# Performance work log

Measured on AMD Instinct MI355X. Metric: run time of the kernel, lower is better.

The kernel has to match this reference:

```python
import jax, jax.numpy as jnp
import numpy as np

def setup_inputs() -> dict:
    key = jax.random.key(0)
    k1, k2 = jax.random.split(key)
    N, M, D = 4096, 4096, 1024
    set1 = jax.random.normal(k1, (N, D), dtype=jnp.float32)
    set2 = jax.random.normal(k2, (M, D), dtype=jnp.float32)
    return {"set1": set1, "set2": set2}

def _l2_dist(x, y):
    # mean over D of squared differences, computed via the expanded GEMM form
    D = x.shape[-1]
    x2 = jnp.sum(x * x, axis=-1)          # [N]
    y2 = jnp.sum(y * y, axis=-1)          # [M]
    xy = jnp.einsum('nd,md->nm', x, y)    # [N, M]
    return (x2[:, None] - 2.0 * xy + y2[None, :]) / D

def reference(set1, set2):
    dist = _l2_dist(set1, set2)                 # [N, M]
    t1 = jnp.mean(jnp.min(dist, axis=1))        # nearest set2 point per set1 point
    t2 = jnp.mean(jnp.min(dist, axis=0))        # nearest set1 point per set2 point
    return (t1 + t2) * 0.5
```

## Files before the change

### kernel.cpp

```cpp
#include <hip/hip_runtime.h>
#include <hip/hip_bf16.h>
#include <stdint.h>


#define NPTS 4096
#define MPTS 4096
#define DDIM 1024

typedef __attribute__((ext_vector_type(8))) short bf16x8;
typedef __attribute__((ext_vector_type(4))) float f32x4;
typedef __attribute__((ext_vector_type(4))) unsigned short us4;

__device__ __forceinline__ unsigned short f2bf(float f) {
    unsigned int u = __float_as_uint(f);
    unsigned int r = 0x7FFFu + ((u >> 16) & 1u);
    return (unsigned short)((u + r) >> 16);
}

__device__ __forceinline__ void gl_lds16(const void* g, void* l) {
    __builtin_amdgcn_global_load_lds(
        (const __attribute__((address_space(1))) unsigned int*)g,
        (__attribute__((address_space(3))) unsigned int*)l, 16, 0, 0);
}

__global__ __launch_bounds__(256) void prepass_kernel(
    const float* __restrict__ s1, const float* __restrict__ s2,
    unsigned short* __restrict__ b1, unsigned short* __restrict__ b2,
    float* __restrict__ norms, unsigned int* __restrict__ mins) {
    const int row = blockIdx.x * 4 + (threadIdx.x >> 6);
    const int lane = threadIdx.x & 63;
    const float* src;
    unsigned short* dst;
    if (row < NPTS) { src = s1 + (size_t)row * DDIM; dst = b1 + (size_t)row * DDIM; }
    else            { src = s2 + (size_t)(row - NPTS) * DDIM; dst = b2 + (size_t)(row - NPTS) * DDIM; }
    float sq = 0.f;
    #pragma unroll
    for (int i = 0; i < 4; ++i) {
        float4 v = ((const float4*)src)[lane + i * 64];
        sq += v.x * v.x + v.y * v.y + v.z * v.z + v.w * v.w;
        us4 o;
        o.x = f2bf(v.x); o.y = f2bf(v.y); o.z = f2bf(v.z); o.w = f2bf(v.w);
        ((us4*)dst)[lane + i * 64] = o;
    }
    #pragma unroll
    for (int off = 32; off; off >>= 1) sq += __shfl_down(sq, off, 64);
    if (lane == 0) { norms[row] = sq; mins[row] = 0x7f7f7f7fu; }
}


#define STAGE_H(ldsBase, gRowBase, kcol) do {                                   \
    gl_lds16((gRowBase) + (size_t)(wave * 8 + srow) * DDIM + (kcol) + schoff,   \
             ldsb + (ldsBase) + wave * 1024);                                   \
    gl_lds16((gRowBase) + (size_t)(64 + wave * 8 + srow) * DDIM + (kcol) + schoff, \
             ldsb + (ldsBase) + 8192 + wave * 1024);                            \
} while (0)

#define RD_A(CURB, aq) do {                                                     \
    _Pragma("unroll")                                                           \
    for (int fl_ = 0; fl_ < 4; ++fl_) {                                         \
        const int row_ = wr * 128 + (aq) * 64 + fl_ * 16 + r0;                  \
        af[fl_][0] = *(const bf16x8*)(ldsb + (CURB) + row_ * 128 + ch0);        \
        af[fl_][1] = *(const bf16x8*)(ldsb + (CURB) + row_ * 128 + ch1);        \
    }                                                                           \
} while (0)

#define RD_B(CURB, bq, dst) do {                                                \
    _Pragma("unroll")                                                           \
    for (int fj_ = 0; fj_ < 2; ++fj_) {                                         \
        const int col_ = wc * 64 + (bq) * 32 + fj_ * 16 + r0;                   \
        dst[fj_][0] = *(const bf16x8*)(ldsb + (CURB) + 32768 + col_ * 128 + ch0); \
        dst[fj_][1] = *(const bf16x8*)(ldsb + (CURB) + 32768 + col_ * 128 + ch1); \
    }                                                                           \
} while (0)

#define MFMA_Q(aq, bq, BF)                                                      \
    _Pragma("unroll")                                                           \
    for (int fl_ = 0; fl_ < 4; ++fl_) {                                         \
        _Pragma("unroll")                                                       \
        for (int fj_ = 0; fj_ < 2; ++fj_) {                                     \
            acc[(aq) * 4 + fl_][(bq) * 2 + fj_] =                               \
                __builtin_amdgcn_mfma_f32_16x16x32_bf16(af[fl_][0], BF[fj_][0], \
                    acc[(aq) * 4 + fl_][(bq) * 2 + fj_], 0, 0, 0);              \
            acc[(aq) * 4 + fl_][(bq) * 2 + fj_] =                               \
                __builtin_amdgcn_mfma_f32_16x16x32_bf16(af[fl_][1], BF[fj_][1], \
                    acc[(aq) * 4 + fl_][(bq) * 2 + fj_], 0, 0, 0);              \
        }                                                                       \
    }

#define BARRIER_MFMA(aq, bq, BF, WAITSTMT) do {                                 \
    __builtin_amdgcn_s_barrier();                                               \
    asm volatile("s_waitcnt lgkmcnt(0)" ::: "memory");                          \
    __builtin_amdgcn_sched_barrier(0);                                          \
    __builtin_amdgcn_s_setprio(1);                                              \
    MFMA_Q(aq, bq, BF);                                                         \
    __builtin_amdgcn_s_setprio(0);                                              \
    WAITSTMT;                                                                   \
    __builtin_amdgcn_s_barrier();                                               \
} while (0)

#define TILE(t, CURB, NXTB) do {                                                \
    const int kN1_ = ((t) + 1) * 64, kN2_ = ((t) + 2) * 64;                     \
    RD_A(CURB, 0); RD_B(CURB, 0, bf0);                                          \
    if ((t) + 1 < 16) STAGE_H((NXTB) + 49152, Bb + 128 * DDIM, kN1_);           \
    BARRIER_MFMA(0, 0, bf0, );                                                  \
    RD_B(CURB, 1, bf1);                                                         \
    if ((t) + 1 < 16) STAGE_H((NXTB) + 16384, Ab + 128 * DDIM, kN1_);           \
    BARRIER_MFMA(0, 1, bf1, );                                                  \
    RD_A(CURB, 1);                                                              \
    if ((t) + 2 < 16) STAGE_H((CURB) + 32768, Bb, kN2_);                        \
    BARRIER_MFMA(1, 1, bf1, );                                                  \
    if ((t) + 2 < 16) STAGE_H((CURB) + 0, Ab, kN2_);                            \
    BARRIER_MFMA(1, 0, bf0,                                                     \
        if ((t) < 14) { asm volatile("s_waitcnt vmcnt(4)" ::: "memory"); }      \
        else if ((t) == 14) { asm volatile("s_waitcnt vmcnt(0)" ::: "memory"); });\
} while (0)

__global__ __launch_bounds__(512, 2) void cham_gemm_kernel(
    const unsigned short* __restrict__ A,
    const unsigned short* __restrict__ B,
    const float* __restrict__ x2, const float* __restrict__ y2,
    unsigned int* __restrict__ mins,
    unsigned int* __restrict__ ctr, float* __restrict__ out) {
    __shared__ __align__(16) char lds[131072];
    char* ldsb = lds;
    unsigned int* rowmin = mins;
    unsigned int* colmin = mins + NPTS;

    const int g = blockIdx.x;
    const int xcd = g & 7;
    const int s = g >> 3;
    const int bi = (xcd >> 1) * 4 + (s >> 3);
    const int bj = (xcd & 1) * 8 + (s & 7);

    const int tid = threadIdx.x;
    const int wave = tid >> 6;
    const int lane = tid & 63;
    const int wr = wave >> 2;
    const int wc = wave & 3;
    const int r0 = lane & 15;
    const int q = lane >> 4;

    const int ch0 = ((q ^ (r0 & 7)) << 4);
    const int ch1 = (((4 + q) ^ (r0 & 7)) << 4);
    const int srow = lane >> 3;
    const int schoff = (((lane & 7) ^ srow) * 8);

    const unsigned short* Ab = A + (size_t)(bi * 256) * DDIM;
    const unsigned short* Bb = B + (size_t)(bj * 256) * DDIM;

    f32x4 acc[8][4];
    #pragma unroll
    for (int i = 0; i < 8; ++i)
        #pragma unroll
        for (int j = 0; j < 4; ++j)
            acc[i][j] = (f32x4){0.f, 0.f, 0.f, 0.f};

    bf16x8 af[4][2], bf0[2][2], bf1[2][2];

    STAGE_H(0 + 32768, Bb, 0);
    STAGE_H(0 + 0, Ab, 0);
    STAGE_H(0 + 49152, Bb + 128 * DDIM, 0);
    STAGE_H(0 + 16384, Ab + 128 * DDIM, 0);
    STAGE_H(65536 + 32768, Bb, 64);
    STAGE_H(65536 + 0, Ab, 64);
    asm volatile("s_waitcnt vmcnt(4)" ::: "memory");
    __builtin_amdgcn_s_barrier();

    for (int tt = 0; tt < 8; ++tt) {
        const int te = 2 * tt, to = 2 * tt + 1;
        TILE(te, 0, 65536);
        TILE(to, 65536, 0);
    }

    const float invD = 1.0f / (float)DDIM;
    const int nb = bi * 256 + wr * 128;
    const int mb = bj * 256 + wc * 64;

    float y2v[4];
    #pragma unroll
    for (int fj = 0; fj < 4; ++fj)
        y2v[fj] = y2[mb + (fj >> 1) * 32 + (fj & 1) * 16 + r0];

    float cv[4];
    #pragma unroll
    for (int fj = 0; fj < 4; ++fj) cv[fj] = 3.0e38f;

    #pragma unroll
    for (int fi = 0; fi < 8; ++fi) {
        #pragma unroll
        for (int rg = 0; rg < 4; ++rg) {
            const int n = nb + fi * 16 + q * 4 + rg;
            const float x2v = x2[n];
            float rv = 3.0e38f;
            #pragma unroll
            for (int fj = 0; fj < 4; ++fj) {
                float d = (x2v + y2v[fj] - 2.0f * acc[fi][fj][rg]) * invD;
                rv = fminf(rv, d);
                cv[fj] = fminf(cv[fj], d);
            }
            rv = fminf(rv, __shfl_xor(rv, 1, 64));
            rv = fminf(rv, __shfl_xor(rv, 2, 64));
            rv = fminf(rv, __shfl_xor(rv, 4, 64));
            rv = fminf(rv, __shfl_xor(rv, 8, 64));
            if (r0 == 0) atomicMin(&rowmin[n], __float_as_uint(rv));
        }
    }

    #pragma unroll
    for (int fj = 0; fj < 4; ++fj) {
        float v = cv[fj];
        v = fminf(v, __shfl_xor(v, 16, 64));
        v = fminf(v, __shfl_xor(v, 32, 64));
        if (lane < 16)
            atomicMin(&colmin[mb + (fj >> 1) * 32 + (fj & 1) * 16 + lane],
                      __float_as_uint(v));
    }

    __syncthreads();
    __shared__ unsigned int lastflag;
    if (tid == 0)
        lastflag = __hip_atomic_fetch_add(&ctr[0], 1u, __ATOMIC_ACQUIRE,
                                          __HIP_MEMORY_SCOPE_AGENT);
    __syncthreads();
    if (lastflag == 255u) {
        float sum = 0.f;
        #pragma unroll
        for (int i = 0; i < 16; ++i)
            sum += __uint_as_float(__hip_atomic_load(&mins[tid + i * 512],
                    __ATOMIC_RELAXED, __HIP_MEMORY_SCOPE_AGENT));
        #pragma unroll
        for (int off = 32; off; off >>= 1) sum += __shfl_down(sum, off, 64);
        float* red = (float*)(ldsb + 64);
        if (lane == 0) red[wave] = sum;
        __syncthreads();
        if (tid == 0) {
            float tot = 0.f;
            #pragma unroll
            for (int i = 0; i < 8; ++i) tot += red[i];
            out[0] = tot * (1.0f / 8192.0f);
        }
    }
}

extern "C" void kernel_launch(void* const* d_in, const int* in_sizes, int n_in,
                              void* d_out, int out_size, void* d_ws, size_t ws_size,
                              hipStream_t stream) {
    const float* s1 = (const float*)d_in[0];
    const float* s2 = (const float*)d_in[1];
    char* ws = (char*)d_ws;

    unsigned short* b1 = (unsigned short*)ws;
    unsigned short* b2 = (unsigned short*)(ws + 8388608);
    float* norms       = (float*)(ws + 16777216);
    unsigned int* mins = (unsigned int*)(ws + 16777216 + 32768);
    unsigned int* ctr  = (unsigned int*)(ws + 16777216 + 65536);
    float* out = (float*)d_out;

    hipMemsetAsync(ctr, 0, 4, stream);
    prepass_kernel<<<2048, 256, 0, stream>>>(s1, s2, b1, b2, norms, mins);
    cham_gemm_kernel<<<256, 512, 0, stream>>>(b1, b2, norms, norms + NPTS,
                                              mins, ctr, out);
}
```

Measured before the change: 130.4 us.

## Switch GEMM to FP8 MFMA with 128x256 tiles and triple-buffered LDS

Inputs are quantized to FP8 instead of BF16 in the prepass, and the distance GEMM uses fp8 MFMA instructions, halving operand bytes. Block tiles shrink to 128x256 with a three-buffer LDS ring, giving 512 blocks and higher occupancy. The separate memset of the completion counter is folded into the prepass kernel, and the XCD-aware block swizzle is dropped. FP8 quantization of the dot products costs accuracy and may push the result past tolerance.

```diff
diff --git a/kernel.cpp b/kernel.cpp
--- a/kernel.cpp
+++ b/kernel.cpp
@@ -7,15 +7,7 @@
 #define MPTS 4096
 #define DDIM 1024
 
-typedef __attribute__((ext_vector_type(8))) short bf16x8;
 typedef __attribute__((ext_vector_type(4))) float f32x4;
-typedef __attribute__((ext_vector_type(4))) unsigned short us4;
-
-__device__ __forceinline__ unsigned short f2bf(float f) {
-    unsigned int u = __float_as_uint(f);
-    unsigned int r = 0x7FFFu + ((u >> 16) & 1u);
-    return (unsigned short)((u + r) >> 16);
-}
 
 __device__ __forceinline__ void gl_lds16(const void* g, void* l) {
     __builtin_amdgcn_global_load_lds(
@@ -25,22 +17,24 @@
 
 __global__ __launch_bounds__(256) void prepass_kernel(
     const float* __restrict__ s1, const float* __restrict__ s2,
-    unsigned short* __restrict__ b1, unsigned short* __restrict__ b2,
-    float* __restrict__ norms, unsigned int* __restrict__ mins) {
+    unsigned char* __restrict__ a8, unsigned char* __restrict__ b8,
+    float* __restrict__ norms, unsigned int* __restrict__ mins,
+    unsigned int* __restrict__ ctr) {
     const int row = blockIdx.x * 4 + (threadIdx.x >> 6);
     const int lane = threadIdx.x & 63;
+    if (blockIdx.x == 0 && threadIdx.x == 0) ctr[0] = 0u;
     const float* src;
-    unsigned short* dst;
-    if (row < NPTS) { src = s1 + (size_t)row * DDIM; dst = b1 + (size_t)row * DDIM; }
-    else            { src = s2 + (size_t)(row - NPTS) * DDIM; dst = b2 + (size_t)(row - NPTS) * DDIM; }
+    unsigned char* dst;
+    if (row < NPTS) { src = s1 + (size_t)row * DDIM; dst = a8 + (size_t)row * DDIM; }
+    else            { src = s2 + (size_t)(row - NPTS) * DDIM; dst = b8 + (size_t)(row - NPTS) * DDIM; }
     float sq = 0.f;
     #pragma unroll
     for (int i = 0; i < 4; ++i) {
         float4 v = ((const float4*)src)[lane + i * 64];
         sq += v.x * v.x + v.y * v.y + v.z * v.z + v.w * v.w;
-        us4 o;
-        o.x = f2bf(v.x); o.y = f2bf(v.y); o.z = f2bf(v.z); o.w = f2bf(v.w);
-        ((us4*)dst)[lane + i * 64] = o;
+        int p = __builtin_amdgcn_cvt_pk_fp8_f32(v.x, v.y, 0, false);
+        p = __builtin_amdgcn_cvt_pk_fp8_f32(v.z, v.w, p, true);
+        ((int*)dst)[lane + i * 64] = p;
     }
     #pragma unroll
     for (int off = 32; off; off >>= 1) sq += __shfl_down(sq, off, 64);
@@ -48,19 +42,33 @@
 }
 
 
-#define STAGE_H(ldsBase, gRowBase, kcol) do {                                   \
-    gl_lds16((gRowBase) + (size_t)(wave * 8 + srow) * DDIM + (kcol) + schoff,   \
-             ldsb + (ldsBase) + wave * 1024);                                   \
-    gl_lds16((gRowBase) + (size_t)(64 + wave * 8 + srow) * DDIM + (kcol) + schoff, \
-             ldsb + (ldsBase) + 8192 + wave * 1024);                            \
+#define BUF0 0
+#define BUF1 24576
+#define BUF2 49152
+
+#define STAGE_A(bufB, kcol) do {                                                \
+    gl_lds16(Ab + (size_t)(wave * 16 + (lane >> 2)) * DDIM + (kcol)             \
+                 + (((lane & 3) ^ ((lane >> 2) & 3)) * 16),                     \
+             ldsb + (bufB) + wave * 1024);                                      \
+} while (0)
+
+#define STAGE_B1(bufB, kcol) do {                                               \
+    gl_lds16(Bb + (size_t)(wave * 16 + (lane >> 2)) * DDIM + (kcol)             \
+                 + (((lane & 3) ^ ((lane >> 2) & 3)) * 16),                     \
+             ldsb + (bufB) + 8192 + wave * 1024);                               \
+} while (0)
+#define STAGE_B2(bufB, kcol) do {                                               \
+    gl_lds16(Bb + (size_t)(128 + wave * 16 + (lane >> 2)) * DDIM + (kcol)       \
+                 + (((lane & 3) ^ ((lane >> 2) & 3)) * 16),                     \
+             ldsb + (bufB) + 8192 + 8192 + wave * 1024);                        \
 } while (0)
 
 #define RD_A(CURB, aq) do {                                                     \
     _Pragma("unroll")                                                           \
-    for (int fl_ = 0; fl_ < 4; ++fl_) {                                         \
-        const int row_ = wr * 128 + (aq) * 64 + fl_ * 16 + r0;                  \
-        af[fl_][0] = *(const bf16x8*)(ldsb + (CURB) + row_ * 128 + ch0);        \
-        af[fl_][1] = *(const bf16x8*)(ldsb + (CURB) + row_ * 128 + ch1);        \
+    for (int fl_ = 0; fl_ < 2; ++fl_) {                                         \
+        const int row_ = wr * 64 + (aq) * 32 + fl_ * 16 + r0;                   \
+        af[fl_][0] = *(const long*)(ldsb + (CURB) + row_ * 64 + ch0);           \
+        af[fl_][1] = *(const long*)(ldsb + (CURB) + row_ * 64 + ch1);           \
     }                                                                           \
 } while (0)
 
@@ -68,22 +76,22 @@
     _Pragma("unroll")                                                           \
     for (int fj_ = 0; fj_ < 2; ++fj_) {                                         \
         const int col_ = wc * 64 + (bq) * 32 + fj_ * 16 + r0;                   \
-        dst[fj_][0] = *(const bf16x8*)(ldsb + (CURB) + 32768 + col_ * 128 + ch0); \
-        dst[fj_][1] = *(const bf16x8*)(ldsb + (CURB) + 32768 + col_ * 128 + ch1); \
+        dst[fj_][0] = *(const long*)(ldsb + (CURB) + 8192 + col_ * 64 + ch0);   \
+        dst[fj_][1] = *(const long*)(ldsb + (CURB) + 8192 + col_ * 64 + ch1);   \
     }                                                                           \
 } while (0)
 
 #define MFMA_Q(aq, bq, BF)                                                      \
     _Pragma("unroll")                                                           \
-    for (int fl_ = 0; fl_ < 4; ++fl_) {                                         \
+    for (int fl_ = 0; fl_ < 2; ++fl_) {                                         \
         _Pragma("unroll")                                                       \
         for (int fj_ = 0; fj_ < 2; ++fj_) {                                     \
-            acc[(aq) * 4 + fl_][(bq) * 2 + fj_] =                               \
-                __builtin_amdgcn_mfma_f32_16x16x32_bf16(af[fl_][0], BF[fj_][0], \
-                    acc[(aq) * 4 + fl_][(bq) * 2 + fj_], 0, 0, 0);              \
-            acc[(aq) * 4 + fl_][(bq) * 2 + fj_] =                               \
-                __builtin_amdgcn_mfma_f32_16x16x32_bf16(af[fl_][1], BF[fj_][1], \
-                    acc[(aq) * 4 + fl_][(bq) * 2 + fj_], 0, 0, 0);              \
+            acc[(aq) * 2 + fl_][(bq) * 2 + fj_] =                               \
+                __builtin_amdgcn_mfma_f32_16x16x32_fp8_fp8(af[fl_][0], BF[fj_][0], \
+                    acc[(aq) * 2 + fl_][(bq) * 2 + fj_], 0, 0, 0);              \
+            acc[(aq) * 2 + fl_][(bq) * 2 + fj_] =                               \
+                __builtin_amdgcn_mfma_f32_16x16x32_fp8_fp8(af[fl_][1], BF[fj_][1], \
+                    acc[(aq) * 2 + fl_][(bq) * 2 + fj_], 0, 0, 0);              \
         }                                                                       \
     }
 
@@ -99,39 +107,34 @@
 } while (0)
 
 #define TILE(t, CURB, NXTB) do {                                                \
-    const int kN1_ = ((t) + 1) * 64, kN2_ = ((t) + 2) * 64;                     \
+    const int kN_ = ((t) + 2) * 64;                                             \
     RD_A(CURB, 0); RD_B(CURB, 0, bf0);                                          \
-    if ((t) + 1 < 16) STAGE_H((NXTB) + 49152, Bb + 128 * DDIM, kN1_);           \
+    if ((t) + 2 < 16) STAGE_A(NXTB, kN_);                                       \
     BARRIER_MFMA(0, 0, bf0, );                                                  \
     RD_B(CURB, 1, bf1);                                                         \
-    if ((t) + 1 < 16) STAGE_H((NXTB) + 16384, Ab + 128 * DDIM, kN1_);           \
+    if ((t) + 2 < 16) STAGE_B1(NXTB, kN_);                                      \
     BARRIER_MFMA(0, 1, bf1, );                                                  \
     RD_A(CURB, 1);                                                              \
-    if ((t) + 2 < 16) STAGE_H((CURB) + 32768, Bb, kN2_);                        \
+    if ((t) + 2 < 16) STAGE_B2(NXTB, kN_);                                      \
     BARRIER_MFMA(1, 1, bf1, );                                                  \
-    if ((t) + 2 < 16) STAGE_H((CURB) + 0, Ab, kN2_);                            \
     BARRIER_MFMA(1, 0, bf0,                                                     \
-        if ((t) < 14) { asm volatile("s_waitcnt vmcnt(4)" ::: "memory"); }      \
+        if ((t) <= 13) { asm volatile("s_waitcnt vmcnt(3)" ::: "memory"); }     \
         else if ((t) == 14) { asm volatile("s_waitcnt vmcnt(0)" ::: "memory"); });\
 } while (0)
 
-__global__ __launch_bounds__(512, 2) void cham_gemm_kernel(
-    const unsigned short* __restrict__ A,
-    const unsigned short* __restrict__ B,
+__global__ __launch_bounds__(512, 4) void cham_gemm_kernel(
+    const unsigned char* __restrict__ A,
+    const unsigned char* __restrict__ B,
     const float* __restrict__ x2, const float* __restrict__ y2,
     unsigned int* __restrict__ mins,
     unsigned int* __restrict__ ctr, float* __restrict__ out) {
-    __shared__ __align__(16) char lds[131072];
+    __shared__ __align__(16) char lds[73728];
     char* ldsb = lds;
     unsigned int* rowmin = mins;
     unsigned int* colmin = mins + NPTS;
 
-    const int g = blockIdx.x;
-    const int xcd = g & 7;
-    const int s = g >> 3;
-    const int bi = (xcd >> 1) * 4 + (s >> 3);
-    const int bj = (xcd & 1) * 8 + (s & 7);
-
+    const int bi = blockIdx.x >> 4;
+    const int bj = blockIdx.x & 15;
     const int tid = threadIdx.x;
     const int wave = tid >> 6;
     const int lane = tid & 63;
@@ -140,53 +143,49 @@
     const int r0 = lane & 15;
     const int q = lane >> 4;
 
-    const int ch0 = ((q ^ (r0 & 7)) << 4);
-    const int ch1 = (((4 + q) ^ (r0 & 7)) << 4);
-    const int srow = lane >> 3;
-    const int schoff = (((lane & 7) ^ srow) * 8);
-
-    const unsigned short* Ab = A + (size_t)(bi * 256) * DDIM;
-    const unsigned short* Bb = B + (size_t)(bj * 256) * DDIM;
-
-    f32x4 acc[8][4];
-    #pragma unroll
-    for (int i = 0; i < 8; ++i)
+    const int ch0 = (((q >> 1) ^ (r0 & 3)) << 4) + ((q & 1) << 3);
+    const int ch1 = (((2 + (q >> 1)) ^ (r0 & 3)) << 4) + ((q & 1) << 3);
+
+    const unsigned char* Ab = A + (size_t)(bi * 128) * DDIM;
+    const unsigned char* Bb = B + (size_t)(bj * 256) * DDIM;
+
+    f32x4 acc[4][4];
+    #pragma unroll
+    for (int i = 0; i < 4; ++i)
         #pragma unroll
         for (int j = 0; j < 4; ++j)
             acc[i][j] = (f32x4){0.f, 0.f, 0.f, 0.f};
 
-    bf16x8 af[4][2], bf0[2][2], bf1[2][2];
-
-    STAGE_H(0 + 32768, Bb, 0);
-    STAGE_H(0 + 0, Ab, 0);
-    STAGE_H(0 + 49152, Bb + 128 * DDIM, 0);
-    STAGE_H(0 + 16384, Ab + 128 * DDIM, 0);
-    STAGE_H(65536 + 32768, Bb, 64);
-    STAGE_H(65536 + 0, Ab, 64);
-    asm volatile("s_waitcnt vmcnt(4)" ::: "memory");
+    long af[2][2], bf0[2][2], bf1[2][2];
+
+    STAGE_A(BUF0, 0); STAGE_B1(BUF0, 0); STAGE_B2(BUF0, 0);
+    STAGE_A(BUF1, 64); STAGE_B1(BUF1, 64); STAGE_B2(BUF1, 64);
+    asm volatile("s_waitcnt vmcnt(3)" ::: "memory");
     __builtin_amdgcn_s_barrier();
 
-    for (int tt = 0; tt < 8; ++tt) {
-        const int te = 2 * tt, to = 2 * tt + 1;
-        TILE(te, 0, 65536);
-        TILE(to, 65536, 0);
-    }
+    #pragma unroll 1
+    for (int tt = 0; tt < 5; ++tt) {
+        const int t3 = 3 * tt;
+        TILE(t3 + 0, BUF0, BUF2);
+        TILE(t3 + 1, BUF1, BUF0);
+        TILE(t3 + 2, BUF2, BUF1);
+    }
+    TILE(15, BUF0, BUF2);
 
     const float invD = 1.0f / (float)DDIM;
-    const int nb = bi * 256 + wr * 128;
+    const int nb = bi * 128 + wr * 64;
     const int mb = bj * 256 + wc * 64;
 
     float y2v[4];
     #pragma unroll
-    for (int fj = 0; fj < 4; ++fj)
-        y2v[fj] = y2[mb + (fj >> 1) * 32 + (fj & 1) * 16 + r0];
+    for (int fj = 0; fj < 4; ++fj) y2v[fj] = y2[mb + fj * 16 + r0];
 
     float cv[4];
     #pragma unroll
     for (int fj = 0; fj < 4; ++fj) cv[fj] = 3.0e38f;
 
     #pragma unroll
-    for (int fi = 0; fi < 8; ++fi) {
+    for (int fi = 0; fi < 4; ++fi) {
         #pragma unroll
         for (int rg = 0; rg < 4; ++rg) {
             const int n = nb + fi * 16 + q * 4 + rg;
@@ -212,8 +211,7 @@
         v = fminf(v, __shfl_xor(v, 16, 64));
         v = fminf(v, __shfl_xor(v, 32, 64));
         if (lane < 16)
-            atomicMin(&colmin[mb + (fj >> 1) * 32 + (fj & 1) * 16 + lane],
-                      __float_as_uint(v));
+            atomicMin(&colmin[mb + fj * 16 + lane], __float_as_uint(v));
     }
 
     __syncthreads();
@@ -222,7 +220,7 @@
         lastflag = __hip_atomic_fetch_add(&ctr[0], 1u, __ATOMIC_ACQUIRE,
                                           __HIP_MEMORY_SCOPE_AGENT);
     __syncthreads();
-    if (lastflag == 255u) {
+    if (lastflag == 511u) {
         float sum = 0.f;
         #pragma unroll
         for (int i = 0; i < 16; ++i)
@@ -230,7 +228,7 @@
                     __ATOMIC_RELAXED, __HIP_MEMORY_SCOPE_AGENT));
         #pragma unroll
         for (int off = 32; off; off >>= 1) sum += __shfl_down(sum, off, 64);
-        float* red = (float*)(ldsb + 64);
+        float* red = (float*)ldsb;
         if (lane == 0) red[wave] = sum;
         __syncthreads();
         if (tid == 0) {
@@ -249,15 +247,14 @@
     const float* s2 = (const float*)d_in[1];
     char* ws = (char*)d_ws;
 
-    unsigned short* b1 = (unsigned short*)ws;
-    unsigned short* b2 = (unsigned short*)(ws + 8388608);
-    float* norms       = (float*)(ws + 16777216);
-    unsigned int* mins = (unsigned int*)(ws + 16777216 + 32768);
-    unsigned int* ctr  = (unsigned int*)(ws + 16777216 + 65536);
+    unsigned char* a8  = (unsigned char*)ws;
+    unsigned char* b8  = (unsigned char*)(ws + 4194304);
+    float* norms       = (float*)(ws + 8388608);
+    unsigned int* mins = (unsigned int*)(ws + 8388608 + 32768);
+    unsigned int* ctr  = (unsigned int*)(ws + 8388608 + 65536);
     float* out = (float*)d_out;
 
-    hipMemsetAsync(ctr, 0, 4, stream);
-    prepass_kernel<<<2048, 256, 0, stream>>>(s1, s2, b1, b2, norms, mins);
-    cham_gemm_kernel<<<256, 512, 0, stream>>>(b1, b2, norms, norms + NPTS,
+    prepass_kernel<<<2048, 256, 0, stream>>>(s1, s2, a8, b8, norms, mins, ctr);
+    cham_gemm_kernel<<<512, 512, 0, stream>>>(a8, b8, norms, norms + NPTS,
                                               mins, ctr, out);
 }
```

Result: slower. 134.5 us (+3.1%).
